# Optimization experiments

Measured on AMD Instinct MI355X. Metric: run time of the kernel, lower is better.

The kernel has to match this reference:

```python
import jax, jax.numpy as jnp
import numpy as np
import math

HID = 128      # hidden_dim == d_inner (expand=1)
NSTATE = 8     # d_state
K = 4          # scan directions
RANK = math.ceil(HID / 16)  # dt_rank = 8
B, H, W = 4, 64, 64


def _ln(x, g, b, eps=1e-5):
    m = jnp.mean(x, -1, keepdims=True)
    v = jnp.mean((x - m) ** 2, -1, keepdims=True)
    return (x - m) * jax.lax.rsqrt(v + eps) * g + b


def _ss2d(x, in_w, conv_w, conv_b, xproj_w, dt_w, dt_b, A_logs, Ds, ln_g, ln_b, out_w):
    # x: [B,H,W,C] -> VMamba SS2D with d_inner=C, 4-direction selective scan
    Bn, Hh, Ww, C = x.shape
    D, L = C, Hh * Ww
    N = A_logs.shape[-1]
    R = dt_w.shape[-1]
    xz = x @ in_w.T                      # [B,H,W,2D]
    xc, z = jnp.split(xz, 2, axis=-1)
    xc = xc.transpose(0, 3, 1, 2)        # [B,D,H,W]
    xc = jax.lax.conv_general_dilated(xc, conv_w, (1, 1), 'SAME', feature_group_count=D)
    xc = jax.nn.silu(xc + conv_b[None, :, None, None])
    x_hw = xc.reshape(Bn, D, L)
    x_wh = xc.transpose(0, 1, 3, 2).reshape(Bn, D, L)
    xs = jnp.stack([x_hw, x_wh, x_hw[..., ::-1], x_wh[..., ::-1]], 1)  # [B,K,D,L]
    x_dbl = jnp.einsum('bkdl,kcd->bkcl', xs, xproj_w)
    dts, Bs, Cs = x_dbl[:, :, :R], x_dbl[:, :, R:R + N], x_dbl[:, :, R + N:]
    dt = jax.nn.softplus(jnp.einsum('bkrl,kdr->bkdl', dts, dt_w) + dt_b[None, :, :, None])
    A = -jnp.exp(A_logs.reshape(K, D, N))  # [K,D,N]

    def step(h, inp):
        x_t, dt_t, B_t, C_t = inp          # [B,K,D],[B,K,D],[B,K,N],[B,K,N]
        h = h * jnp.exp(dt_t[..., None] * A) + dt_t[..., None] * B_t[:, :, None, :] * x_t[..., None]
        return h, jnp.einsum('bkdn,bkn->bkd', h, C_t)

    h0 = jnp.zeros((Bn, K, D, N), x.dtype)
    _, ys = jax.lax.scan(step, h0, (xs.transpose(3, 0, 1, 2), dt.transpose(3, 0, 1, 2),
                                    Bs.transpose(3, 0, 1, 2), Cs.transpose(3, 0, 1, 2)))
    out_y = ys.transpose(1, 2, 3, 0) + Ds.reshape(K, D)[None, :, :, None] * xs  # [B,K,D,L]
    wh_y = out_y[:, 3, :, ::-1].reshape(Bn, D, Ww, Hh).transpose(0, 1, 3, 2).reshape(Bn, D, L)
    invwh_y = out_y[:, 1].reshape(Bn, D, Ww, Hh).transpose(0, 1, 3, 2).reshape(Bn, D, L)
    y = out_y[:, 0] + out_y[:, 2, :, ::-1] + wh_y + invwh_y
    y = _ln(y.transpose(0, 2, 1).reshape(Bn, Hh, Ww, D), ln_g, ln_b)
    return (y * jax.nn.silu(z)) @ out_w.T


def _enhance(x, g, b, w, bias):
    return jax.nn.gelu(_ln(x, g, b) @ w.T + bias, approximate=False)


def setup_inputs() -> dict:
    key = jax.random.key(0)
    ks = jax.random.split(key, 12)
    f = lambda k, s, sc=0.02: jax.random.normal(k, s, jnp.float32) * sc
    return dict(
        sar_feat=jax.random.normal(ks[0], (B, H, W, HID), jnp.float32),
        opt_feat=jax.random.normal(ks[1], (B, H, W, HID), jnp.float32),
        ss_in_w=f(ks[2], (2, 2 * HID, HID)),
        ss_conv_w=f(ks[3], (2, HID, 1, 3, 3), 0.1),
        ss_conv_b=f(ks[4], (2, HID)),
        ss_xproj_w=f(ks[5], (2, K, RANK + 2 * NSTATE, HID)),
        ss_dt_w=f(ks[6], (2, K, HID, RANK), 0.1),
        ss_dt_b=f(ks[7], (2, K, HID), 0.1),
        ss_Alogs=jnp.tile(jnp.log(jnp.arange(1, NSTATE + 1, dtype=jnp.float32)), (2, K * HID, 1)),
        ss_Ds=jnp.ones((2, K * HID), jnp.float32),
        ss_ln_g=jnp.ones((2, HID), jnp.float32),
        ss_ln_b=jnp.zeros((2, HID), jnp.float32),
        ss_out_w=f(ks[8], (2, HID, HID)),
        enh_ln_g=jnp.ones((2, HID), jnp.float32),
        enh_ln_b=jnp.zeros((2, HID), jnp.float32),
        enh_w=f(ks[9], (2, HID, HID)),
        enh_b=jnp.zeros((2, HID), jnp.float32),
    )


def reference(sar_feat, opt_feat, ss_in_w, ss_conv_w, ss_conv_b, ss_xproj_w, ss_dt_w,
              ss_dt_b, ss_Alogs, ss_Ds, ss_ln_g, ss_ln_b, ss_out_w,
              enh_ln_g, enh_ln_b, enh_w, enh_b):
    # cat([opt,sar],-1)[...,:C] == opt ; cat([sar,opt],-1)[...,:C] == sar (faithful identity slice)
    # index 0 = cross_ss2d_s2o (input opt), index 1 = cross_ss2d_o2s (input sar)
    xin = jnp.stack([opt_feat, sar_feat])
    guided = jax.vmap(_ss2d)(xin, ss_in_w, ss_conv_w, ss_conv_b, ss_xproj_w, ss_dt_w,
                             ss_dt_b, ss_Alogs, ss_Ds, ss_ln_g, ss_ln_b, ss_out_w)
    # enhance params: index 0 = enhance_sar (on sar_guided=guided[1]), index 1 = enhance_opt (on opt_guided=guided[0])
    enh_in = jnp.stack([guided[1], guided[0]])
    enhanced = jax.vmap(_enhance)(enh_in, enh_ln_g, enh_ln_b, enh_w, enh_b)
    return (sar_feat + enhanced[0], opt_feat + enhanced[1])
```

## Files before the change

kernel.cpp:

```cpp
#include <hip/hip_runtime.h>
#include <hip/hip_bf16.h>
#include <math.h>

#define DEV __device__ __forceinline__

static constexpr int LL = 4096;
static constexpr int DD = 128;
static constexpr int SEG = 128;
static constexpr float LOG2E = 1.4426950408889634f;
static constexpr float LN2 = 0.6931471805599453f;

DEV float silu_(float x) { return x / (1.f + __expf(-x)); }
DEV float erf_(float x) {
  const float ax = fabsf(x);
  const float t = 1.f / fmaf(0.3275911f, ax, 1.f);
  float p = fmaf(1.061405429f, t, -1.453152027f);
  p = fmaf(p, t, 1.421413741f);
  p = fmaf(p, t, -0.284496736f);
  p = fmaf(p, t, 0.254829592f);
  p = p * t;
  const float r = 1.f - p * __expf(-ax * ax);
  return x < 0.f ? -r : r;
}
DEV float gelu_(float x) { return 0.5f * x * (1.f + erf_(x * 0.7071067811865475f)); }
DEV float sp_(float x) {
  const float t = __builtin_amdgcn_exp2f(-fabsf(x) * LOG2E);
  return fmaxf(x, 0.f) + LN2 * __builtin_amdgcn_logf(1.f + t);
}

template <int CTRL>
DEV float dpp_add_(float x) {
  int y = __builtin_amdgcn_update_dpp(0, __float_as_int(x), CTRL, 0xF, 0xF, true);
  return x + __int_as_float(y);
}

DEV void seg_base_step(int k, int s, int& base, int& step) {
  if (k == 0)      { base = s * 64;        step = 1;   }
  else if (k == 1) { base = s;             step = 64;  }
  else if (k == 2) { base = 4095 - s * 64; step = -1;  }
  else             { base = 4095 - s;      step = -64; }
}

__global__ __launch_bounds__(256) void k_inproj(
    const float* __restrict__ sar, const float* __restrict__ opt,
    const float* __restrict__ in_w, float* __restrict__ xz) {
  const int lt = blockIdx.x, ct = blockIdx.y, mb = blockIdx.z;
  const int m = mb >> 2;
  const float* __restrict__ x = (m == 0 ? opt : sar) + (size_t)(mb & 3) * (LL * DD);
  const float* __restrict__ W = in_w + (size_t)m * 256 * DD;
  __shared__ float sA[64][68];
  __shared__ float sW[64][68];
  const int tid = threadIdx.x;
  const int tc = tid & 15, tl = tid >> 4;
  float acc[4][4] = {};
  for (int db = 0; db < 2; ++db) {
    __syncthreads();
    for (int idx = tid; idx < 64 * 16; idx += 256) {
      const int r = idx >> 4, d4 = (idx & 15) << 2;
      *(float4*)&sA[r][d4] = *(const float4*)&x[(size_t)(lt * 64 + r) * DD + db * 64 + d4];
      *(float4*)&sW[r][d4] = *(const float4*)&W[(size_t)(ct * 64 + r) * DD + db * 64 + d4];
    }
    __syncthreads();
#pragma unroll 4
    for (int d = 0; d < 64; d += 4) {
      float4 a[4], w[4];
#pragma unroll
      for (int q = 0; q < 4; ++q) a[q] = *(const float4*)&sA[tl * 4 + q][d];
#pragma unroll
      for (int j = 0; j < 4; ++j) w[j] = *(const float4*)&sW[tc + 16 * j][d];
#pragma unroll
      for (int j = 0; j < 4; ++j)
#pragma unroll
        for (int q = 0; q < 4; ++q)
          acc[j][q] += a[q].x * w[j].x + a[q].y * w[j].y + a[q].z * w[j].z + a[q].w * w[j].w;
    }
  }
  float* __restrict__ dst = xz + ((size_t)mb * 256 + ct * 64) * LL + lt * 64;
#pragma unroll
  for (int j = 0; j < 4; ++j) {
    float4 v = make_float4(acc[j][0], acc[j][1], acc[j][2], acc[j][3]);
    *(float4*)&dst[(size_t)(tc + 16 * j) * LL + tl * 4] = v;
  }
}

__global__ __launch_bounds__(256) void k_conv(
    const float* __restrict__ xz, const float* __restrict__ conv_w,
    const float* __restrict__ conv_b, float* __restrict__ xc) {
  const int ht = blockIdx.x, dg = blockIdx.y, mb = blockIdx.z;
  const int m = mb >> 2;
  __shared__ float sIn[8][18][66];
  __shared__ float sOut[1024][8];
  const float* __restrict__ src = xz + ((size_t)mb * 256 + dg * 8) * LL;
  const int tid = threadIdx.x;
  for (int idx = tid; idx < 8 * 18 * 66; idx += 256) {
    const int dd = idx / (18 * 66);
    const int rem = idx - dd * (18 * 66);
    const int hh = rem / 66, ww = rem - hh * 66;
    const int h = ht * 16 + hh - 1, w = ww - 1;
    float v = 0.f;
    if (h >= 0 && h < 64 && w >= 0 && w < 64) v = src[(size_t)dd * LL + h * 64 + w];
    sIn[dd][hh][ww] = v;
  }
  __syncthreads();
  const int dd = tid & 7, wv = tid >> 3;
  const int dch = dg * 8 + dd;
  float wk[9];
#pragma unroll
  for (int t = 0; t < 9; ++t) wk[t] = conv_w[((size_t)m * DD + dch) * 9 + t];
  const float bias = conv_b[m * DD + dch];
  for (int hh = 0; hh < 16; ++hh) {
#pragma unroll
    for (int wh = 0; wh < 2; ++wh) {
      const int w = wv + wh * 32;
      float s = bias;
#pragma unroll
      for (int kh = 0; kh < 3; ++kh)
#pragma unroll
        for (int kw = 0; kw < 3; ++kw)
          s = fmaf(sIn[dd][hh + kh][w + kw], wk[kh * 3 + kw], s);
      sOut[hh * 64 + w][dd] = silu_(s);
    }
  }
  __syncthreads();
  float* __restrict__ dst = xc + (size_t)mb * LL * DD + dg * 8;
#pragma unroll
  for (int r = 0; r < 4; ++r) {
    const int pos = tid + r * 256;
    const int l = ht * 1024 + pos;
    *(float4*)&dst[(size_t)l * DD + 0] = *(const float4*)&sOut[pos][0];
    *(float4*)&dst[(size_t)l * DD + 4] = *(const float4*)&sOut[pos][4];
  }
}

__global__ __launch_bounds__(256) void k_xproj(
    const float* __restrict__ xc, const float* __restrict__ xproj_w,
    float* __restrict__ xdbl) {
  const int lt = blockIdx.x, k = blockIdx.y, mb = blockIdx.z;
  const int m = mb >> 2, mbk = mb * 4 + k;
  __shared__ float sX[64][132];
  __shared__ float sW[24][132];
  const int tid = threadIdx.x;
  const float* __restrict__ src = xc + (size_t)mb * LL * DD;
  int base, step;
  seg_base_step(k, lt, base, step);
  for (int idx = tid; idx < 64 * 32; idx += 256) {
    const int l = idx >> 5, d4 = (idx & 31) << 2;
    *(float4*)&sX[l][d4] = *(const float4*)&src[(size_t)(base + l * step) * DD + d4];
  }
  const float* __restrict__ Wsrc = xproj_w + ((size_t)m * 4 + k) * 24 * DD;
  for (int idx = tid; idx < 24 * 32; idx += 256) {
    const int r = idx >> 5, d4 = (idx & 31) << 2;
    *(float4*)&sW[r][d4] = *(const float4*)&Wsrc[(size_t)r * DD + d4];
  }
  __syncthreads();
  const int l = tid >> 2, cg = tid & 3;
  float acc[6] = {};
#pragma unroll 8
  for (int d = 0; d < 128; d += 4) {
    const float4 xv = *(const float4*)&sX[l][d];
#pragma unroll
    for (int j = 0; j < 6; ++j) {
      const float4 wv = *(const float4*)&sW[cg * 6 + j][d];
      acc[j] += xv.x * wv.x + xv.y * wv.y + xv.z * wv.z + xv.w * wv.w;
    }
  }
  float* __restrict__ dst = xdbl + ((size_t)mbk * LL + lt * 64 + l) * 24 + cg * 6;
#pragma unroll
  for (int j = 0; j < 6; ++j) dst[j] = acc[j];
}


DEV void load_aln2(const float* __restrict__ Alogs, int m, int k, int d,
                   float* __restrict__ aln2, bool& fastp) {
  const float4 a0 = *(const float4*)&Alogs[((size_t)m * 512 + k * DD + d) * 8];
  const float4 a1 = *(const float4*)&Alogs[((size_t)m * 512 + k * DD + d) * 8 + 4];
  aln2[0] = -__expf(a0.x) * LOG2E; aln2[1] = -__expf(a0.y) * LOG2E;
  aln2[2] = -__expf(a0.z) * LOG2E; aln2[3] = -__expf(a0.w) * LOG2E;
  aln2[4] = -__expf(a1.x) * LOG2E; aln2[5] = -__expf(a1.y) * LOG2E;
  aln2[6] = -__expf(a1.z) * LOG2E; aln2[7] = -__expf(a1.w) * LOG2E;
  fastp = true;
#pragma unroll
  for (int n = 1; n < 8; ++n)
    fastp = fastp && (fabsf(aln2[n] - (float)(n + 1) * aln2[0]) <=
                      1e-4f * fabsf(aln2[n]) + 1e-12f);
}

DEV void load_w8(const float* __restrict__ dt_w, int mbk, int d,
                 float* __restrict__ wreg) {
  const float4 w0 = *(const float4*)&dt_w[((size_t)mbk * DD + d) * 8];
  const float4 w1 = *(const float4*)&dt_w[((size_t)mbk * DD + d) * 8 + 4];
  wreg[0] = w0.x; wreg[1] = w0.y; wreg[2] = w0.z; wreg[3] = w0.w;
  wreg[4] = w1.x; wreg[5] = w1.y; wreg[6] = w1.z; wreg[7] = w1.w;
}

template <bool FAST>
DEV void qpow_(float dt, const float* __restrict__ aln2, float* __restrict__ q) {
  if constexpr (FAST) {
    q[0] = __builtin_amdgcn_exp2f(dt * aln2[0]);
    q[1] = q[0] * q[0]; q[2] = q[1] * q[0]; q[3] = q[1] * q[1];
    q[4] = q[3] * q[0]; q[5] = q[3] * q[1]; q[6] = q[3] * q[2]; q[7] = q[3] * q[3];
  } else {
#pragma unroll
    for (int n = 0; n < 8; ++n) q[n] = __builtin_amdgcn_exp2f(dt * aln2[n]);
  }
}

DEV float dt_of_(const float* __restrict__ t24,
                 const float* __restrict__ w, float bw) {
  const float4 t0 = *(const float4*)&t24[0];
  const float4 t1 = *(const float4*)&t24[4];
  float s = bw;
  s = fmaf(t0.x, w[0], s); s = fmaf(t0.y, w[1], s);
  s = fmaf(t0.z, w[2], s); s = fmaf(t0.w, w[3], s);
  s = fmaf(t1.x, w[4], s); s = fmaf(t1.y, w[5], s);
  s = fmaf(t1.z, w[6], s); s = fmaf(t1.w, w[7], s);
  return sp_(s);
}

template <bool FAST>
DEV void hstep_(const float* __restrict__ t24, float dt, float x,
                const float* __restrict__ aln2, float* __restrict__ h) {
  const float u = dt * x;
  float q[8];
  qpow_<FAST>(dt, aln2, q);
  const float4 b0 = *(const float4*)&t24[8];
  const float4 b1 = *(const float4*)&t24[12];
  h[0] = fmaf(h[0], q[0], u * b0.x);
  h[1] = fmaf(h[1], q[1], u * b0.y);
  h[2] = fmaf(h[2], q[2], u * b0.z);
  h[3] = fmaf(h[3], q[3], u * b0.w);
  h[4] = fmaf(h[4], q[4], u * b1.x);
  h[5] = fmaf(h[5], q[5], u * b1.y);
  h[6] = fmaf(h[6], q[6], u * b1.z);
  h[7] = fmaf(h[7], q[7], u * b1.w);
}

template <bool FAST>
DEV float ystep_(const float* __restrict__ t24, float dt, float x,
                 const float* __restrict__ aln2, float dsv,
                 float* __restrict__ h) {
  const float u = dt * x;
  float q[8];
  qpow_<FAST>(dt, aln2, q);
  const float4 b0 = *(const float4*)&t24[8];
  const float4 b1 = *(const float4*)&t24[12];
  const float4 c0 = *(const float4*)&t24[16];
  const float4 c1 = *(const float4*)&t24[20];
  float y = dsv * x;
  h[0] = fmaf(h[0], q[0], u * b0.x); y = fmaf(h[0], c0.x, y);
  h[1] = fmaf(h[1], q[1], u * b0.y); y = fmaf(h[1], c0.y, y);
  h[2] = fmaf(h[2], q[2], u * b0.z); y = fmaf(h[2], c0.z, y);
  h[3] = fmaf(h[3], q[3], u * b0.w); y = fmaf(h[3], c0.w, y);
  h[4] = fmaf(h[4], q[4], u * b1.x); y = fmaf(h[4], c1.x, y);
  h[5] = fmaf(h[5], q[5], u * b1.y); y = fmaf(h[5], c1.y, y);
  h[6] = fmaf(h[6], q[6], u * b1.z); y = fmaf(h[6], c1.z, y);
  h[7] = fmaf(h[7], q[7], u * b1.w); y = fmaf(h[7], c1.w, y);
  return y;
}

template <bool FAST>
DEV void loop1d_(const float* __restrict__ tA, const float* __restrict__ tB,
                 const float* __restrict__ sx, int d,
                 const float* __restrict__ aln2A, const float* __restrict__ aln2B,
                 const float* __restrict__ wA, const float* __restrict__ wB,
                 float bwA, float bwB, float* __restrict__ hA,
                 float* __restrict__ hB, float& dtsA, float& dtsB) {
#pragma unroll 8
  for (int j = 0; j < 32; ++j) {
    const float xA = sx[j * 128 + d];
    const float xB = sx[(31 - j) * 128 + d];
    const float dtA = dt_of_(tA + j * 24, wA, bwA);
    const float dtB = dt_of_(tB + j * 24, wB, bwB);
    dtsA += dtA; dtsB += dtB;
    hstep_<FAST>(tA + j * 24, dtA, xA, aln2A, hA);
    hstep_<FAST>(tB + j * 24, dtB, xB, aln2B, hB);
  }
}

__global__ __launch_bounds__(128) void k_scan1(
    const float* __restrict__ xc, const float* __restrict__ xdbl,
    const float* __restrict__ dt_w, const float* __restrict__ dt_b,
    const float* __restrict__ Alogs, float* __restrict__ hend,
    float* __restrict__ Pseg) {
  const int s = blockIdx.x, p = blockIdx.y, mb = blockIdx.z;
  const int m = mb >> 2;
  const int kA = p, kB = p + 2;
  const int sA = s, sB = 127 - s;
  const int mbkA = mb * 4 + kA, mbkB = mb * 4 + kB;
  const int d = threadIdx.x;
  __shared__ float sx[32 * 128];

  const float* __restrict__ tA = xdbl + ((size_t)mbkA * LL + sA * 32) * 24;
  const float* __restrict__ tB = xdbl + ((size_t)mbkB * LL + sB * 32) * 24;

  const int base0 = (p == 0) ? s * 32 : ((s & 1) * 32) * 64 + (s >> 1);
  const int stepPos = (p == 0) ? 1 : 64;
  const float* __restrict__ xsrc = xc + (size_t)mb * LL * DD;
#pragma unroll
  for (int t = 0; t < 8; ++t) {
    const int idx = d + t * 128;
    const int r = idx >> 5, c4 = (idx & 31) << 2;
    ((float4*)sx)[idx] = *(const float4*)&xsrc[(size_t)(base0 + r * stepPos) * DD + c4];
  }

  float aln2A[8], aln2B[8]; bool fA, fB;
  load_aln2(Alogs, m, kA, d, aln2A, fA);
  load_aln2(Alogs, m, kB, d, aln2B, fB);
  float wA[8], wB[8];
  load_w8(dt_w, mbkA, d, wA);
  load_w8(dt_w, mbkB, d, wB);
  const float bwA = dt_b[(size_t)mbkA * DD + d];
  const float bwB = dt_b[(size_t)mbkB * DD + d];
  __syncthreads();

  float hA[8] = {0, 0, 0, 0, 0, 0, 0, 0};
  float hB[8] = {0, 0, 0, 0, 0, 0, 0, 0};
  float dtsA = 0.f, dtsB = 0.f;
  if (fA && fB)
    loop1d_<true>(tA, tB, sx, d, aln2A, aln2B, wA, wB, bwA, bwB, hA, hB, dtsA, dtsB);
  else
    loop1d_<false>(tA, tB, sx, d, aln2A, aln2B, wA, wB, bwA, bwB, hA, hB, dtsA, dtsB);

  {
    float* __restrict__ he = hend + (((size_t)mbkA * SEG + sA) << 10) + d * 8;
    float* __restrict__ pe = Pseg + (((size_t)mbkA * SEG + sA) << 10) + d * 8;
    *(float4*)&he[0] = make_float4(hA[0], hA[1], hA[2], hA[3]);
    *(float4*)&he[4] = make_float4(hA[4], hA[5], hA[6], hA[7]);
    *(float4*)&pe[0] = make_float4(
        __builtin_amdgcn_exp2f(aln2A[0] * dtsA), __builtin_amdgcn_exp2f(aln2A[1] * dtsA),
        __builtin_amdgcn_exp2f(aln2A[2] * dtsA), __builtin_amdgcn_exp2f(aln2A[3] * dtsA));
    *(float4*)&pe[4] = make_float4(
        __builtin_amdgcn_exp2f(aln2A[4] * dtsA), __builtin_amdgcn_exp2f(aln2A[5] * dtsA),
        __builtin_amdgcn_exp2f(aln2A[6] * dtsA), __builtin_amdgcn_exp2f(aln2A[7] * dtsA));
  }
  {
    float* __restrict__ he = hend + (((size_t)mbkB * SEG + sB) << 10) + d * 8;
    float* __restrict__ pe = Pseg + (((size_t)mbkB * SEG + sB) << 10) + d * 8;
    *(float4*)&he[0] = make_float4(hB[0], hB[1], hB[2], hB[3]);
    *(float4*)&he[4] = make_float4(hB[4], hB[5], hB[6], hB[7]);
    *(float4*)&pe[0] = make_float4(
        __builtin_amdgcn_exp2f(aln2B[0] * dtsB), __builtin_amdgcn_exp2f(aln2B[1] * dtsB),
        __builtin_amdgcn_exp2f(aln2B[2] * dtsB), __builtin_amdgcn_exp2f(aln2B[3] * dtsB));
    *(float4*)&pe[4] = make_float4(
        __builtin_amdgcn_exp2f(aln2B[4] * dtsB), __builtin_amdgcn_exp2f(aln2B[5] * dtsB),
        __builtin_amdgcn_exp2f(aln2B[6] * dtsB), __builtin_amdgcn_exp2f(aln2B[7] * dtsB));
  }
}

__global__ __launch_bounds__(256) void k_scan2(
    const float* __restrict__ hend, const float* __restrict__ Pseg,
    float* __restrict__ hin) {
  const int gid = blockIdx.x * 256 + threadIdx.x;
  const int mbk = gid >> 10, dn = gid & 1023;
  const float* __restrict__ P = Pseg + ((size_t)mbk * SEG << 10) + dn;
  const float* __restrict__ E = hend + ((size_t)mbk * SEG << 10) + dn;
  float* __restrict__ O = hin + ((size_t)mbk * SEG << 10) + dn;
  float h = 0.f;
  for (int c0 = 0; c0 < SEG; c0 += 16) {
    float pv[16], ev[16];
#pragma unroll
    for (int t = 0; t < 16; ++t) {
      pv[t] = P[(size_t)(c0 + t) << 10];
      ev[t] = E[(size_t)(c0 + t) << 10];
    }
#pragma unroll
    for (int t = 0; t < 16; ++t) {
      O[(size_t)(c0 + t) << 10] = h;
      h = fmaf(pv[t], h, ev[t]);
    }
  }
}

template <bool FAST>
DEV void chainA_(const float* __restrict__ t24, const float* __restrict__ sx, int d,
                 const float* __restrict__ aln2, const float* __restrict__ w,
                 float bw, float dsv, float* __restrict__ h,
                 float* __restrict__ va) {
#pragma unroll
  for (int j = 0; j < 32; ++j) {
    const float x = sx[j * 128 + d];
    const float dt = dt_of_(t24 + j * 24, w, bw);
    va[j] = ystep_<FAST>(t24 + j * 24, dt, x, aln2, dsv, h);
  }
}

template <bool FAST>
DEV void chainB_(const float* __restrict__ t24, const float* __restrict__ sx, int d,
                 const float* __restrict__ aln2, const float* __restrict__ w,
                 float bw, float dsv, float* __restrict__ h,
                 const float* __restrict__ va, float* __restrict__ yd,
                 ptrdiff_t sstep) {
#pragma unroll
  for (int j = 0; j < 32; ++j) {
    const int phys = 31 - j;
    const float x = sx[phys * 128 + d];
    const float dt = dt_of_(t24 + j * 24, w, bw);
    const float v = ystep_<FAST>(t24 + j * 24, dt, x, aln2, dsv, h);
    yd[(ptrdiff_t)phys * sstep] = v + va[phys];
  }
}

__global__ __launch_bounds__(128) void k_scan3(
    const float* __restrict__ xc, const float* __restrict__ xdbl,
    const float* __restrict__ dt_w, const float* __restrict__ dt_b,
    const float* __restrict__ Alogs, const float* __restrict__ Ds,
    const float* __restrict__ hin, float* __restrict__ yrow,
    float* __restrict__ ycol) {
  const int s = blockIdx.x, p = blockIdx.y, mb = blockIdx.z;
  const int m = mb >> 2;
  const int kA = p, kB = p + 2;
  const int sA = s, sB = 127 - s;
  const int mbkA = mb * 4 + kA, mbkB = mb * 4 + kB;
  const int d = threadIdx.x;
  __shared__ float sx[32 * 128];

  const float* __restrict__ tA = xdbl + ((size_t)mbkA * LL + sA * 32) * 24;
  const float* __restrict__ tB = xdbl + ((size_t)mbkB * LL + sB * 32) * 24;

  const int base0 = (p == 0) ? s * 32 : ((s & 1) * 32) * 64 + (s >> 1);
  const int stepPos = (p == 0) ? 1 : 64;
  const float* __restrict__ xsrc = xc + (size_t)mb * LL * DD;
#pragma unroll
  for (int t = 0; t < 8; ++t) {
    const int idx = d + t * 128;
    const int r = idx >> 5, c4 = (idx & 31) << 2;
    ((float4*)sx)[idx] = *(const float4*)&xsrc[(size_t)(base0 + r * stepPos) * DD + c4];
  }

  float aln2A[8], aln2B[8]; bool fA, fB;
  load_aln2(Alogs, m, kA, d, aln2A, fA);
  load_aln2(Alogs, m, kB, d, aln2B, fB);
  float wA[8], wB[8];
  load_w8(dt_w, mbkA, d, wA);
  load_w8(dt_w, mbkB, d, wB);
  const float bwA = dt_b[(size_t)mbkA * DD + d];
  const float bwB = dt_b[(size_t)mbkB * DD + d];
  const float dsvA = Ds[(size_t)m * 512 + kA * DD + d];
  const float dsvB = Ds[(size_t)m * 512 + kB * DD + d];

  float hA[8], hB[8];
  {
    const float* hp = hin + (((size_t)mbkA * SEG + sA) << 10) + d * 8;
    const float4 h0 = *(const float4*)&hp[0];
    const float4 h1 = *(const float4*)&hp[4];
    hA[0] = h0.x; hA[1] = h0.y; hA[2] = h0.z; hA[3] = h0.w;
    hA[4] = h1.x; hA[5] = h1.y; hA[6] = h1.z; hA[7] = h1.w;
  }
  {
    const float* hp = hin + (((size_t)mbkB * SEG + sB) << 10) + d * 8;
    const float4 h0 = *(const float4*)&hp[0];
    const float4 h1 = *(const float4*)&hp[4];
    hB[0] = h0.x; hB[1] = h0.y; hB[2] = h0.z; hB[3] = h0.w;
    hB[4] = h1.x; hB[5] = h1.y; hB[6] = h1.z; hB[7] = h1.w;
  }

  const size_t off0 = (size_t)mb * LL * DD + (size_t)base0 * DD + d;
  float* __restrict__ yd = (p == 0 ? yrow : ycol) + off0;
  const ptrdiff_t sstep = (ptrdiff_t)stepPos * DD;
  __syncthreads();

  float va[32];
  if (fA) chainA_<true>(tA, sx, d, aln2A, wA, bwA, dsvA, hA, va);
  else    chainA_<false>(tA, sx, d, aln2A, wA, bwA, dsvA, hA, va);
  if (fB) chainB_<true>(tB, sx, d, aln2B, wB, bwB, dsvB, hB, va, yd, sstep);
  else    chainB_<false>(tB, sx, d, aln2B, wB, bwB, dsvB, hB, va, yd, sstep);
}

__global__ __launch_bounds__(256) void k_outproj(
    const float* __restrict__ yrow, const float* __restrict__ ycol,
    const float* __restrict__ xz, const float* __restrict__ ln_g,
    const float* __restrict__ ln_b, const float* __restrict__ out_w,
    float* __restrict__ guided) {
  const int lt = blockIdx.x, mb = blockIdx.y;
  const int m = mb >> 2;
  __shared__ float sv[32][132];
  __shared__ float sW[64][68];
  __shared__ float smr[32][2];
  __shared__ float sg[128], sb[128];
  const int tid = threadIdx.x;
  const size_t yoff = ((size_t)mb * LL + lt * 32) * DD;
  const float4* p0 = (const float4*)(yrow + yoff);
  const float4* p1 = (const float4*)(ycol + yoff);
  float4 ya[4], yb[4];
#pragma unroll
  for (int t = 0; t < 4; ++t) { ya[t] = p0[tid + t * 256]; yb[t] = p1[tid + t * 256]; }
  const int zc = tid >> 1, zh = tid & 1;
  const float4* zsrc = (const float4*)(xz + ((size_t)mb * 256 + 128 + zc) * LL + lt * 32 + zh * 16);
  float4 zv[4];
#pragma unroll
  for (int t = 0; t < 4; ++t) zv[t] = zsrc[t];
  const float* __restrict__ Wp = out_w + (size_t)m * DD * DD;
  float4 wpre[4];
#pragma unroll
  for (int t = 0; t < 4; ++t) {
    const int idx = tid + t * 256;
    wpre[t] = *(const float4*)&Wp[(size_t)(idx >> 4) * DD + ((idx & 15) << 2)];
  }
  if (tid < 128) { sg[tid] = ln_g[m * DD + tid]; sb[tid] = ln_b[m * DD + tid]; }
#pragma unroll
  for (int t = 0; t < 4; ++t) {
    const int idx = tid + t * 256;
    float4 v;
    v.x = ya[t].x + yb[t].x; v.y = ya[t].y + yb[t].y;
    v.z = ya[t].z + yb[t].z; v.w = ya[t].w + yb[t].w;
    *(float4*)&sv[idx >> 5][(idx & 31) << 2] = v;
  }
  __syncthreads();
  {
    const int l = tid >> 3, q = tid & 7;
    float s = 0.f, s2 = 0.f;
#pragma unroll
    for (int d0 = 0; d0 < 16; d0 += 4) {
      const float4 v = *(const float4*)&sv[l][q * 16 + d0];
      s += v.x + v.y + v.z + v.w;
      s2 += v.x * v.x + v.y * v.y + v.z * v.z + v.w * v.w;
    }
    s = dpp_add_<0xB1>(s); s = dpp_add_<0x4E>(s); s = dpp_add_<0x141>(s);
    s2 = dpp_add_<0xB1>(s2); s2 = dpp_add_<0x4E>(s2); s2 = dpp_add_<0x141>(s2);
    if (q == 0) {
      const float mean = s * (1.f / 128.f);
      smr[l][0] = mean;
      smr[l][1] = rsqrtf(fmaf(s2, 1.f / 128.f, -mean * mean) + 1e-5f);
    }
  }
  __syncthreads();
  {
    const float g = sg[zc], bb = sb[zc];
    const float* zf = (const float*)zv;
#pragma unroll
    for (int i2 = 0; i2 < 16; ++i2) {
      const int l = zh * 16 + i2;
      const float v = fmaf((sv[l][zc] - smr[l][0]) * smr[l][1], g, bb);
      sv[l][zc] = v * silu_(zf[i2]);
    }
  }
  const int tc = tid & 15, tl = tid >> 4;
  float* __restrict__ dst = guided + ((size_t)mb * LL + lt * 32) * DD;
#pragma unroll
  for (int jb = 0; jb < 2; ++jb) {
    float acc[4][2] = {};
#pragma unroll
    for (int db = 0; db < 2; ++db) {
      __syncthreads();
#pragma unroll
      for (int t = 0; t < 4; ++t) {
        const int idx = tid + t * 256;
        *(float4*)&sW[idx >> 4][(idx & 15) << 2] = wpre[t];
      }
      const int ph = jb * 2 + db + 1;
      if (ph < 4) {
        const int jb2 = ph >> 1, db2 = ph & 1;
#pragma unroll
        for (int t = 0; t < 4; ++t) {
          const int idx = tid + t * 256;
          wpre[t] = *(const float4*)&Wp[(size_t)(jb2 * 64 + (idx >> 4)) * DD + db2 * 64 + ((idx & 15) << 2)];
        }
      }
      __syncthreads();
#pragma unroll 4
      for (int d0 = 0; d0 < 64; d0 += 4) {
        float4 av[2], wv[4];
#pragma unroll
        for (int q = 0; q < 2; ++q) av[q] = *(const float4*)&sv[tl * 2 + q][db * 64 + d0];
#pragma unroll
        for (int j = 0; j < 4; ++j) wv[j] = *(const float4*)&sW[tc + 16 * j][d0];
#pragma unroll
        for (int j = 0; j < 4; ++j)
#pragma unroll
          for (int q = 0; q < 2; ++q)
            acc[j][q] += av[q].x * wv[j].x + av[q].y * wv[j].y + av[q].z * wv[j].z + av[q].w * wv[j].w;
      }
    }
#pragma unroll
    for (int j = 0; j < 4; ++j)
#pragma unroll
      for (int q = 0; q < 2; ++q)
        dst[(size_t)(tl * 2 + q) * DD + jb * 64 + tc + 16 * j] = acc[j][q];
  }
}

__global__ __launch_bounds__(256) void k_enhance(
    const float* __restrict__ guided, const float* __restrict__ eg,
    const float* __restrict__ ebv, const float* __restrict__ ew,
    const float* __restrict__ ebias, const float* __restrict__ sar,
    const float* __restrict__ opt, float* __restrict__ outp) {
  const int lt = blockIdx.x, ib = blockIdx.y;
  const int i = ib >> 2, b = ib & 3;
  __shared__ float sv[32][132];
  __shared__ float sW[64][68];
  __shared__ float smr[32][2];
  __shared__ float sg[128], sb2[128], sbias[128];
  const int tid = threadIdx.x;
  const float4* gsrc =
      (const float4*)(guided + (((size_t)(1 - i) * 4 + b) * LL + lt * 32) * DD);
  float4 gv[4];
#pragma unroll
  for (int t = 0; t < 4; ++t) gv[t] = gsrc[tid + t * 256];
  const float* __restrict__ Wp = ew + (size_t)i * DD * DD;
  float4 wpre[4];
#pragma unroll
  for (int t = 0; t < 4; ++t) {
    const int idx = tid + t * 256;
    wpre[t] = *(const float4*)&Wp[(size_t)(idx >> 4) * DD + ((idx & 15) << 2)];
  }
  if (tid < 128) {
    sg[tid] = eg[i * DD + tid];
    sb2[tid] = ebv[i * DD + tid];
    sbias[tid] = ebias[i * DD + tid];
  }
#pragma unroll
  for (int t = 0; t < 4; ++t) {
    const int idx = tid + t * 256;
    *(float4*)&sv[idx >> 5][(idx & 31) << 2] = gv[t];
  }
  __syncthreads();
  {
    const int l = tid >> 3, q = tid & 7;
    float s = 0.f, s2 = 0.f;
#pragma unroll
    for (int d0 = 0; d0 < 16; d0 += 4) {
      const float4 v = *(const float4*)&sv[l][q * 16 + d0];
      s += v.x + v.y + v.z + v.w;
      s2 += v.x * v.x + v.y * v.y + v.z * v.z + v.w * v.w;
    }
    s = dpp_add_<0xB1>(s); s = dpp_add_<0x4E>(s); s = dpp_add_<0x141>(s);
    s2 = dpp_add_<0xB1>(s2); s2 = dpp_add_<0x4E>(s2); s2 = dpp_add_<0x141>(s2);
    if (q == 0) {
      const float mean = s * (1.f / 128.f);
      smr[l][0] = mean;
      smr[l][1] = rsqrtf(fmaf(s2, 1.f / 128.f, -mean * mean) + 1e-5f);
    }
  }
  __syncthreads();
  {
    const int c = tid >> 1, half = tid & 1;
    const float g = sg[c], bb = sb2[c];
#pragma unroll
    for (int i2 = 0; i2 < 16; ++i2) {
      const int l = half * 16 + i2;
      sv[l][c] = fmaf((sv[l][c] - smr[l][0]) * smr[l][1], g, bb);
    }
  }
  const int tc = tid & 15, tl = tid >> 4;
  const float* __restrict__ resid = (i == 0 ? sar : opt) + ((size_t)b * LL + lt * 32) * DD;
  float* __restrict__ dst = outp + (size_t)i * (4 * LL * DD) + ((size_t)b * LL + lt * 32) * DD;
  float rv[16];
#pragma unroll
  for (int jb = 0; jb < 2; ++jb)
#pragma unroll
    for (int j = 0; j < 4; ++j)
#pragma unroll
      for (int q = 0; q < 2; ++q)
        rv[jb * 8 + j * 2 + q] = resid[(size_t)(tl * 2 + q) * DD + jb * 64 + tc + 16 * j];
  float accA[4][2] = {}, accB[4][2] = {};
#pragma unroll
  for (int jb = 0; jb < 2; ++jb) {
#pragma unroll
    for (int db = 0; db < 2; ++db) {
      __syncthreads();
#pragma unroll
      for (int t = 0; t < 4; ++t) {
        const int idx = tid + t * 256;
        *(float4*)&sW[idx >> 4][(idx & 15) << 2] = wpre[t];
      }
      const int ph = jb * 2 + db + 1;
      if (ph < 4) {
        const int jb2 = ph >> 1, db2 = ph & 1;
#pragma unroll
        for (int t = 0; t < 4; ++t) {
          const int idx = tid + t * 256;
          wpre[t] = *(const float4*)&Wp[(size_t)(jb2 * 64 + (idx >> 4)) * DD + db2 * 64 + ((idx & 15) << 2)];
        }
      }
      __syncthreads();
      float (*acc)[2] = (jb == 0) ? accA : accB;
#pragma unroll 4
      for (int d0 = 0; d0 < 64; d0 += 4) {
        float4 av[2], wv[4];
#pragma unroll
        for (int q = 0; q < 2; ++q) av[q] = *(const float4*)&sv[tl * 2 + q][db * 64 + d0];
#pragma unroll
        for (int j = 0; j < 4; ++j) wv[j] = *(const float4*)&sW[tc + 16 * j][d0];
#pragma unroll
        for (int j = 0; j < 4; ++j)
#pragma unroll
          for (int q = 0; q < 2; ++q)
            acc[j][q] += av[q].x * wv[j].x + av[q].y * wv[j].y + av[q].z * wv[j].z + av[q].w * wv[j].w;
      }
    }
  }
#pragma unroll
  for (int jb = 0; jb < 2; ++jb)
#pragma unroll
    for (int j = 0; j < 4; ++j)
#pragma unroll
      for (int q = 0; q < 2; ++q) {
        const int col = jb * 64 + tc + 16 * j;
        const float u = ((jb == 0) ? accA[j][q] : accB[j][q]) + sbias[col];
        dst[(size_t)(tl * 2 + q) * DD + col] = rv[jb * 8 + j * 2 + q] + gelu_(u);
      }
}

extern "C" void kernel_launch(void* const* d_in, const int* in_sizes, int n_in,
                              void* d_out, int out_size, void* d_ws, size_t ws_size,
                              hipStream_t stream) {
  (void)in_sizes; (void)n_in; (void)out_size; (void)ws_size;
  const float* sar    = (const float*)d_in[0];
  const float* opt    = (const float*)d_in[1];
  const float* in_w   = (const float*)d_in[2];
  const float* conv_w = (const float*)d_in[3];
  const float* conv_b = (const float*)d_in[4];
  const float* xproj_w= (const float*)d_in[5];
  const float* dt_w   = (const float*)d_in[6];
  const float* dt_b   = (const float*)d_in[7];
  const float* Alogs  = (const float*)d_in[8];
  const float* Ds     = (const float*)d_in[9];
  const float* ln_g   = (const float*)d_in[10];
  const float* ln_b   = (const float*)d_in[11];
  const float* out_w  = (const float*)d_in[12];
  const float* eg     = (const float*)d_in[13];
  const float* eb     = (const float*)d_in[14];
  const float* ew     = (const float*)d_in[15];
  const float* ebias  = (const float*)d_in[16];

  float* ws     = (float*)d_ws;
  float* xz     = ws;
  float* xc     = xz + 8388608;
  float* xdbl   = xc + 4194304;
  float* yrowb  = xdbl + 3145728;
  float* ycolb  = yrowb + 4194304;
  float* guided = ycolb + 4194304;
  float* hend   = guided + 4194304;
  float* Pseg   = hend + 4194304;
  float* hin    = Pseg + 4194304;
  float* outf   = (float*)d_out;

  k_inproj <<<dim3(64, 4, 8), 256, 0, stream>>>(sar, opt, in_w, xz);
  k_conv   <<<dim3(4, 16, 8), 256, 0, stream>>>(xz, conv_w, conv_b, xc);
  k_xproj  <<<dim3(64, 4, 8), 256, 0, stream>>>(xc, xproj_w, xdbl);
  k_scan1  <<<dim3(128, 2, 8), 128, 0, stream>>>(xc, xdbl, dt_w, dt_b, Alogs, hend, Pseg);
  k_scan2  <<<dim3(128), 256, 0, stream>>>(hend, Pseg, hin);
  k_scan3  <<<dim3(128, 2, 8), 128, 0, stream>>>(xc, xdbl, dt_w, dt_b, Alogs, Ds, hin,
                                                 yrowb, ycolb);
  k_outproj<<<dim3(128, 8), 256, 0, stream>>>(yrowb, ycolb, xz, ln_g, ln_b, out_w, guided);
  k_enhance<<<dim3(128, 8), 256, 0, stream>>>(guided, eg, eb, ew, ebias, sar, opt, outf);
}
```

Baseline: 265.4 us.

## Use bf16 MFMA for in/out/enhance projections and pair reversed xproj directions

Replaces the FP32 shared-memory tiled GEMMs in the input projection, output projection and enhance kernels with bf16 MFMA 16x16x32 instructions. Operands are converted from global or shared fp32 on the fly, and the weight staging in shared memory is dropped. The xproj kernel now computes direction k and its reversed partner k+2 from one loaded tile, halving the grid and the input reads. This trades fp32 precision for bf16 rounding in three GEMMs and adds uncoalesced strided stores in inproj.

New measurement: 242.8 us. 1.09x faster.

```diff
diff --git a/kernel.cpp b/kernel.cpp
--- a/kernel.cpp
+++ b/kernel.cpp
@@ -9,6 +9,9 @@
 static constexpr int SEG = 128;
 static constexpr float LOG2E = 1.4426950408889634f;
 static constexpr float LN2 = 0.6931471805599453f;
+
+typedef short bf16x8 __attribute__((ext_vector_type(8)));
+typedef float f32x4 __attribute__((ext_vector_type(4)));
 
 DEV float silu_(float x) { return x / (1.f + __expf(-x)); }
 DEV float erf_(float x) {
@@ -34,6 +37,18 @@
   return x + __int_as_float(y);
 }
 
+DEV short f2bf(float f) {
+  unsigned u = __float_as_uint(f);
+  u += 0x7FFF + ((u >> 16) & 1);
+  return (short)(u >> 16);
+}
+DEV bf16x8 cvt8(float4 a, float4 b) {
+  bf16x8 r;
+  r[0] = f2bf(a.x); r[1] = f2bf(a.y); r[2] = f2bf(a.z); r[3] = f2bf(a.w);
+  r[4] = f2bf(b.x); r[5] = f2bf(b.y); r[6] = f2bf(b.z); r[7] = f2bf(b.w);
+  return r;
+}
+
 DEV void seg_base_step(int k, int s, int& base, int& step) {
   if (k == 0)      { base = s * 64;        step = 1;   }
   else if (k == 1) { base = s;             step = 64;  }
@@ -47,40 +62,31 @@
   const int lt = blockIdx.x, ct = blockIdx.y, mb = blockIdx.z;
   const int m = mb >> 2;
   const float* __restrict__ x = (m == 0 ? opt : sar) + (size_t)(mb & 3) * (LL * DD);
-  const float* __restrict__ W = in_w + (size_t)m * 256 * DD;
-  __shared__ float sA[64][68];
-  __shared__ float sW[64][68];
+  const float* __restrict__ W = in_w + (size_t)m * 256 * DD + (size_t)ct * 64 * DD;
   const int tid = threadIdx.x;
-  const int tc = tid & 15, tl = tid >> 4;
-  float acc[4][4] = {};
-  for (int db = 0; db < 2; ++db) {
-    __syncthreads();
-    for (int idx = tid; idx < 64 * 16; idx += 256) {
-      const int r = idx >> 4, d4 = (idx & 15) << 2;
-      *(float4*)&sA[r][d4] = *(const float4*)&x[(size_t)(lt * 64 + r) * DD + db * 64 + d4];
-      *(float4*)&sW[r][d4] = *(const float4*)&W[(size_t)(ct * 64 + r) * DD + db * 64 + d4];
-    }
-    __syncthreads();
-#pragma unroll 4
-    for (int d = 0; d < 64; d += 4) {
-      float4 a[4], w[4];
-#pragma unroll
-      for (int q = 0; q < 4; ++q) a[q] = *(const float4*)&sA[tl * 4 + q][d];
-#pragma unroll
-      for (int j = 0; j < 4; ++j) w[j] = *(const float4*)&sW[tc + 16 * j][d];
-#pragma unroll
-      for (int j = 0; j < 4; ++j)
-#pragma unroll
-        for (int q = 0; q < 4; ++q)
-          acc[j][q] += a[q].x * w[j].x + a[q].y * w[j].y + a[q].z * w[j].z + a[q].w * w[j].w;
-    }
-  }
-  float* __restrict__ dst = xz + ((size_t)mb * 256 + ct * 64) * LL + lt * 64;
-#pragma unroll
-  for (int j = 0; j < 4; ++j) {
-    float4 v = make_float4(acc[j][0], acc[j][1], acc[j][2], acc[j][3]);
-    *(float4*)&dst[(size_t)(tc + 16 * j) * LL + tl * 4] = v;
-  }
+  const int lane = tid & 63, wv = tid >> 6;
+  const int lr = lane & 15, kg = (lane >> 4) * 8;
+  const int lrow = lt * 64 + wv * 16 + lr;
+  f32x4 acc[4] = {};
+#pragma unroll
+  for (int ks = 0; ks < 4; ++ks) {
+    const int d0 = ks * 32 + kg;
+    const float* __restrict__ xp = x + (size_t)lrow * DD + d0;
+    const bf16x8 bfr = cvt8(*(const float4*)xp, *(const float4*)(xp + 4));
+#pragma unroll
+    for (int ctl = 0; ctl < 4; ++ctl) {
+      const float* __restrict__ wp = W + (size_t)(ctl * 16 + lr) * DD + d0;
+      const bf16x8 afr = cvt8(*(const float4*)wp, *(const float4*)(wp + 4));
+      acc[ctl] = __builtin_amdgcn_mfma_f32_16x16x32_bf16(afr, bfr, acc[ctl], 0, 0, 0);
+    }
+  }
+  const int crow0 = ct * 64 + (lane >> 4) * 4;
+  float* __restrict__ dst = xz + (size_t)mb * 256 * LL + lrow;
+#pragma unroll
+  for (int ctl = 0; ctl < 4; ++ctl)
+#pragma unroll
+    for (int r = 0; r < 4; ++r)
+      dst[(size_t)(crow0 + ctl * 16 + r) * LL] = acc[ctl][r];
 }
 
 __global__ __launch_bounds__(256) void k_conv(
@@ -135,40 +141,47 @@
 __global__ __launch_bounds__(256) void k_xproj(
     const float* __restrict__ xc, const float* __restrict__ xproj_w,
     float* __restrict__ xdbl) {
-  const int lt = blockIdx.x, k = blockIdx.y, mb = blockIdx.z;
-  const int m = mb >> 2, mbk = mb * 4 + k;
+  const int lt = blockIdx.x, p = blockIdx.y, mb = blockIdx.z;
+  const int m = mb >> 2;
+  const int mbkA = mb * 4 + p, mbkB = mb * 4 + p + 2;
   __shared__ float sX[64][132];
-  __shared__ float sW[24][132];
+  __shared__ float sWA[24][132];
+  __shared__ float sWB[24][132];
   const int tid = threadIdx.x;
   const float* __restrict__ src = xc + (size_t)mb * LL * DD;
   int base, step;
-  seg_base_step(k, lt, base, step);
+  seg_base_step(p, lt, base, step);
   for (int idx = tid; idx < 64 * 32; idx += 256) {
     const int l = idx >> 5, d4 = (idx & 31) << 2;
     *(float4*)&sX[l][d4] = *(const float4*)&src[(size_t)(base + l * step) * DD + d4];
   }
-  const float* __restrict__ Wsrc = xproj_w + ((size_t)m * 4 + k) * 24 * DD;
+  const float* __restrict__ WsA = xproj_w + ((size_t)m * 4 + p) * 24 * DD;
+  const float* __restrict__ WsB = xproj_w + ((size_t)m * 4 + p + 2) * 24 * DD;
   for (int idx = tid; idx < 24 * 32; idx += 256) {
     const int r = idx >> 5, d4 = (idx & 31) << 2;
-    *(float4*)&sW[r][d4] = *(const float4*)&Wsrc[(size_t)r * DD + d4];
+    *(float4*)&sWA[r][d4] = *(const float4*)&WsA[(size_t)r * DD + d4];
+    *(float4*)&sWB[r][d4] = *(const float4*)&WsB[(size_t)r * DD + d4];
   }
   __syncthreads();
   const int l = tid >> 2, cg = tid & 3;
-  float acc[6] = {};
+  float acc[6] = {}, acc2[6] = {};
 #pragma unroll 8
   for (int d = 0; d < 128; d += 4) {
     const float4 xv = *(const float4*)&sX[l][d];
 #pragma unroll
     for (int j = 0; j < 6; ++j) {
-      const float4 wv = *(const float4*)&sW[cg * 6 + j][d];
-      acc[j] += xv.x * wv.x + xv.y * wv.y + xv.z * wv.z + xv.w * wv.w;
-    }
-  }
-  float* __restrict__ dst = xdbl + ((size_t)mbk * LL + lt * 64 + l) * 24 + cg * 6;
-#pragma unroll
-  for (int j = 0; j < 6; ++j) dst[j] = acc[j];
-}
-
+      const float4 wa = *(const float4*)&sWA[cg * 6 + j][d];
+      const float4 wb = *(const float4*)&sWB[cg * 6 + j][d];
+      acc[j] += xv.x * wa.x + xv.y * wa.y + xv.z * wa.z + xv.w * wa.w;
+      acc2[j] += xv.x * wb.x + xv.y * wb.y + xv.z * wb.z + xv.w * wb.w;
+    }
+  }
+  const int rowA = lt * 64 + l;
+  float* __restrict__ dstA = xdbl + ((size_t)mbkA * LL + rowA) * 24 + cg * 6;
+  float* __restrict__ dstB = xdbl + ((size_t)mbkB * LL + (4095 - rowA)) * 24 + cg * 6;
+#pragma unroll
+  for (int j = 0; j < 6; ++j) { dstA[j] = acc[j]; dstB[j] = acc2[j]; }
+}
 
 DEV void load_aln2(const float* __restrict__ Alogs, int m, int k, int d,
                    float* __restrict__ aln2, bool& fastp) {
@@ -474,7 +487,6 @@
   const int lt = blockIdx.x, mb = blockIdx.y;
   const int m = mb >> 2;
   __shared__ float sv[32][132];
-  __shared__ float sW[64][68];
   __shared__ float smr[32][2];
   __shared__ float sg[128], sb[128];
   const int tid = threadIdx.x;
@@ -489,13 +501,6 @@
   float4 zv[4];
 #pragma unroll
   for (int t = 0; t < 4; ++t) zv[t] = zsrc[t];
-  const float* __restrict__ Wp = out_w + (size_t)m * DD * DD;
-  float4 wpre[4];
-#pragma unroll
-  for (int t = 0; t < 4; ++t) {
-    const int idx = tid + t * 256;
-    wpre[t] = *(const float4*)&Wp[(size_t)(idx >> 4) * DD + ((idx & 15) << 2)];
-  }
   if (tid < 128) { sg[tid] = ln_g[m * DD + tid]; sb[tid] = ln_b[m * DD + tid]; }
 #pragma unroll
   for (int t = 0; t < 4; ++t) {
@@ -534,48 +539,31 @@
       sv[l][zc] = v * silu_(zf[i2]);
     }
   }
-  const int tc = tid & 15, tl = tid >> 4;
-  float* __restrict__ dst = guided + ((size_t)mb * LL + lt * 32) * DD;
-#pragma unroll
-  for (int jb = 0; jb < 2; ++jb) {
-    float acc[4][2] = {};
-#pragma unroll
-    for (int db = 0; db < 2; ++db) {
-      __syncthreads();
-#pragma unroll
-      for (int t = 0; t < 4; ++t) {
-        const int idx = tid + t * 256;
-        *(float4*)&sW[idx >> 4][(idx & 15) << 2] = wpre[t];
-      }
-      const int ph = jb * 2 + db + 1;
-      if (ph < 4) {
-        const int jb2 = ph >> 1, db2 = ph & 1;
-#pragma unroll
-        for (int t = 0; t < 4; ++t) {
-          const int idx = tid + t * 256;
-          wpre[t] = *(const float4*)&Wp[(size_t)(jb2 * 64 + (idx >> 4)) * DD + db2 * 64 + ((idx & 15) << 2)];
-        }
-      }
-      __syncthreads();
-#pragma unroll 4
-      for (int d0 = 0; d0 < 64; d0 += 4) {
-        float4 av[2], wv[4];
-#pragma unroll
-        for (int q = 0; q < 2; ++q) av[q] = *(const float4*)&sv[tl * 2 + q][db * 64 + d0];
-#pragma unroll
-        for (int j = 0; j < 4; ++j) wv[j] = *(const float4*)&sW[tc + 16 * j][d0];
-#pragma unroll
-        for (int j = 0; j < 4; ++j)
-#pragma unroll
-          for (int q = 0; q < 2; ++q)
-            acc[j][q] += av[q].x * wv[j].x + av[q].y * wv[j].y + av[q].z * wv[j].z + av[q].w * wv[j].w;
-      }
-    }
-#pragma unroll
-    for (int j = 0; j < 4; ++j)
-#pragma unroll
-      for (int q = 0; q < 2; ++q)
-        dst[(size_t)(tl * 2 + q) * DD + jb * 64 + tc + 16 * j] = acc[j][q];
+  __syncthreads();
+  const int lane = tid & 63, wv = tid >> 6;
+  const int l0 = (wv & 1) * 16, c0 = (wv >> 1) * 64;
+  const int lr = lane & 15, kg = (lane >> 4) * 8;
+  const float* __restrict__ Wm = out_w + (size_t)m * DD * DD;
+  f32x4 acc[4] = {};
+#pragma unroll
+  for (int ks = 0; ks < 4; ++ks) {
+    const int d0 = ks * 32 + kg;
+    const bf16x8 bfr = cvt8(*(const float4*)&sv[l0 + lr][d0],
+                            *(const float4*)&sv[l0 + lr][d0 + 4]);
+#pragma unroll
+    for (int ctl = 0; ctl < 4; ++ctl) {
+      const float* __restrict__ wp = Wm + (size_t)(c0 + ctl * 16 + lr) * DD + d0;
+      const bf16x8 afr = cvt8(*(const float4*)wp, *(const float4*)(wp + 4));
+      acc[ctl] = __builtin_amdgcn_mfma_f32_16x16x32_bf16(afr, bfr, acc[ctl], 0, 0, 0);
+    }
+  }
+  const int lo = l0 + lr;
+  const int cb = c0 + (lane >> 4) * 4;
+  float* __restrict__ dst = guided + ((size_t)mb * LL + lt * 32 + lo) * DD;
+#pragma unroll
+  for (int ctl = 0; ctl < 4; ++ctl) {
+    float4 v = make_float4(acc[ctl][0], acc[ctl][1], acc[ctl][2], acc[ctl][3]);
+    *(float4*)&dst[cb + ctl * 16] = v;
   }
 }
 
@@ -587,7 +575,6 @@
   const int lt = blockIdx.x, ib = blockIdx.y;
   const int i = ib >> 2, b = ib & 3;
   __shared__ float sv[32][132];
-  __shared__ float sW[64][68];
   __shared__ float smr[32][2];
   __shared__ float sg[128], sb2[128], sbias[128];
   const int tid = threadIdx.x;
@@ -596,13 +583,6 @@
   float4 gv[4];
 #pragma unroll
   for (int t = 0; t < 4; ++t) gv[t] = gsrc[tid + t * 256];
-  const float* __restrict__ Wp = ew + (size_t)i * DD * DD;
-  float4 wpre[4];
-#pragma unroll
-  for (int t = 0; t < 4; ++t) {
-    const int idx = tid + t * 256;
-    wpre[t] = *(const float4*)&Wp[(size_t)(idx >> 4) * DD + ((idx & 15) << 2)];
-  }
   if (tid < 128) {
     sg[tid] = eg[i * DD + tid];
     sb2[tid] = ebv[i * DD + tid];
@@ -641,64 +621,42 @@
       sv[l][c] = fmaf((sv[l][c] - smr[l][0]) * smr[l][1], g, bb);
     }
   }
-  const int tc = tid & 15, tl = tid >> 4;
-  const float* __restrict__ resid = (i == 0 ? sar : opt) + ((size_t)b * LL + lt * 32) * DD;
-  float* __restrict__ dst = outp + (size_t)i * (4 * LL * DD) + ((size_t)b * LL + lt * 32) * DD;
-  float rv[16];
-#pragma unroll
-  for (int jb = 0; jb < 2; ++jb)
-#pragma unroll
-    for (int j = 0; j < 4; ++j)
-#pragma unroll
-      for (int q = 0; q < 2; ++q)
-        rv[jb * 8 + j * 2 + q] = resid[(size_t)(tl * 2 + q) * DD + jb * 64 + tc + 16 * j];
-  float accA[4][2] = {}, accB[4][2] = {};
-#pragma unroll
-  for (int jb = 0; jb < 2; ++jb) {
-#pragma unroll
-    for (int db = 0; db < 2; ++db) {
-      __syncthreads();
-#pragma unroll
-      for (int t = 0; t < 4; ++t) {
-        const int idx = tid + t * 256;
-        *(float4*)&sW[idx >> 4][(idx & 15) << 2] = wpre[t];
-      }
-      const int ph = jb * 2 + db + 1;
-      if (ph < 4) {
-        const int jb2 = ph >> 1, db2 = ph & 1;
-#pragma unroll
-        for (int t = 0; t < 4; ++t) {
-          const int idx = tid + t * 256;
-          wpre[t] = *(const float4*)&Wp[(size_t)(jb2 * 64 + (idx >> 4)) * DD + db2 * 64 + ((idx & 15) << 2)];
-        }
-      }
-      __syncthreads();
-      float (*acc)[2] = (jb == 0) ? accA : accB;
-#pragma unroll 4
-      for (int d0 = 0; d0 < 64; d0 += 4) {
-        float4 av[2], wv[4];
-#pragma unroll
-        for (int q = 0; q < 2; ++q) av[q] = *(const float4*)&sv[tl * 2 + q][db * 64 + d0];
-#pragma unroll
-        for (int j = 0; j < 4; ++j) wv[j] = *(const float4*)&sW[tc + 16 * j][d0];
-#pragma unroll
-        for (int j = 0; j < 4; ++j)
-#pragma unroll
-          for (int q = 0; q < 2; ++q)
-            acc[j][q] += av[q].x * wv[j].x + av[q].y * wv[j].y + av[q].z * wv[j].z + av[q].w * wv[j].w;
-      }
-    }
-  }
-#pragma unroll
-  for (int jb = 0; jb < 2; ++jb)
-#pragma unroll
-    for (int j = 0; j < 4; ++j)
-#pragma unroll
-      for (int q = 0; q < 2; ++q) {
-        const int col = jb * 64 + tc + 16 * j;
-        const float u = ((jb == 0) ? accA[j][q] : accB[j][q]) + sbias[col];
-        dst[(size_t)(tl * 2 + q) * DD + col] = rv[jb * 8 + j * 2 + q] + gelu_(u);
-      }
+  __syncthreads();
+  const int lane = tid & 63, wv = tid >> 6;
+  const int l0 = (wv & 1) * 16, c0 = (wv >> 1) * 64;
+  const int lr = lane & 15, kg = (lane >> 4) * 8;
+  const float* __restrict__ Wm = ew + (size_t)i * DD * DD;
+  f32x4 acc[4] = {};
+#pragma unroll
+  for (int ks = 0; ks < 4; ++ks) {
+    const int d0 = ks * 32 + kg;
+    const bf16x8 bfr = cvt8(*(const float4*)&sv[l0 + lr][d0],
+                            *(const float4*)&sv[l0 + lr][d0 + 4]);
+#pragma unroll
+    for (int ctl = 0; ctl < 4; ++ctl) {
+      const float* __restrict__ wp = Wm + (size_t)(c0 + ctl * 16 + lr) * DD + d0;
+      const bf16x8 afr = cvt8(*(const float4*)wp, *(const float4*)(wp + 4));
+      acc[ctl] = __builtin_amdgcn_mfma_f32_16x16x32_bf16(afr, bfr, acc[ctl], 0, 0, 0);
+    }
+  }
+  const int lo = l0 + lr;
+  const int cb = c0 + (lane >> 4) * 4;
+  const float* __restrict__ resid =
+      (i == 0 ? sar : opt) + ((size_t)b * LL + lt * 32 + lo) * DD;
+  float* __restrict__ dst =
+      outp + (size_t)i * (4 * LL * DD) + ((size_t)b * LL + lt * 32 + lo) * DD;
+#pragma unroll
+  for (int ctl = 0; ctl < 4; ++ctl) {
+    const int c = cb + ctl * 16;
+    const float4 bia = *(const float4*)&sbias[c];
+    const float4 rr = *(const float4*)&resid[c];
+    float4 o;
+    o.x = rr.x + gelu_(acc[ctl][0] + bia.x);
+    o.y = rr.y + gelu_(acc[ctl][1] + bia.y);
+    o.z = rr.z + gelu_(acc[ctl][2] + bia.z);
+    o.w = rr.w + gelu_(acc[ctl][3] + bia.w);
+    *(float4*)&dst[c] = o;
+  }
 }
 
 extern "C" void kernel_launch(void* const* d_in, const int* in_sizes, int n_in,
@@ -737,7 +695,7 @@
 
   k_inproj <<<dim3(64, 4, 8), 256, 0, stream>>>(sar, opt, in_w, xz);
   k_conv   <<<dim3(4, 16, 8), 256, 0, stream>>>(xz, conv_w, conv_b, xc);
-  k_xproj  <<<dim3(64, 4, 8), 256, 0, stream>>>(xc, xproj_w, xdbl);
+  k_xproj  <<<dim3(64, 2, 8), 256, 0, stream>>>(xc, xproj_w, xdbl);
   k_scan1  <<<dim3(128, 2, 8), 128, 0, stream>>>(xc, xdbl, dt_w, dt_b, Alogs, hend, Pseg);
   k_scan2  <<<dim3(128), 256, 0, stream>>>(hend, Pseg, hin);
   k_scan3  <<<dim3(128, 2, 8), 128, 0, stream>>>(xc, xdbl, dt_w, dt_b, Alogs, Ds, hin,
```
